# Performance work log

Hardware: AMD Instinct MI355X
Metric: run time of the kernel (lower is better)

The kernel has to match this reference:

```python
import jax, jax.numpy as jnp
import numpy as np

B, T, C = 4, 2048, 2048
H = 16
DH = C // H  # 128
ROPE_BASE = 10000.0


def _rms_norm(x):
    eps = jnp.finfo(x.dtype).eps
    return x * jax.lax.rsqrt(jnp.mean(x * x, axis=-1, keepdims=True) + eps)


def _rope_tables(seq_len, dim, dtype):
    inv_freq = 1.0 / (ROPE_BASE ** (jnp.arange(0, dim, 2, dtype=jnp.float32) / dim))
    t = jnp.arange(seq_len, dtype=jnp.float32)
    freqs = jnp.outer(t, inv_freq)  # [T, dim/2]
    return jnp.cos(freqs).astype(dtype), jnp.sin(freqs).astype(dtype)


def _apply_rotary(x, cos, sin):
    # x: [B, T, H, DH]; cos/sin: [T, DH/2] broadcast over batch and heads
    d = x.shape[-1] // 2
    x1, x2 = x[..., :d], x[..., d:]
    c = cos[None, :, None, :]
    s = sin[None, :, None, :]
    y1 = x1 * c + x2 * s
    y2 = -x1 * s + x2 * c
    return jnp.concatenate([y1, y2], axis=-1).astype(x.dtype)


def setup_inputs() -> dict:
    key = jax.random.key(0)
    k0, k1, k2, k3, k4 = jax.random.split(key, 5)
    scale = 1.0 / np.sqrt(C)
    return {
        "residual": jax.random.normal(k0, (B, T, C), dtype=jnp.float32),
        "wq": jax.random.normal(k1, (C, C), dtype=jnp.float32) * scale,
        "wk": jax.random.normal(k2, (C, C), dtype=jnp.float32) * scale,
        "wv": jax.random.normal(k3, (C, C), dtype=jnp.float32) * scale,
        "wproj": jax.random.normal(k4, (C, C), dtype=jnp.float32) * scale,
    }


def reference(residual, wq, wk, wv, wproj):
    x = _rms_norm(residual)  # [B, T, C]
    # torch Linear: y = x @ W.T, W is [out, in]
    q = jnp.einsum('btc,dc->btd', x, wq).reshape(B, T, H, DH)
    k = jnp.einsum('btc,dc->btd', x, wk).reshape(B, T, H, DH)
    v = jnp.einsum('btc,dc->btd', x, wv).reshape(B, T, H, DH)
    # per-head QK RMSNorm
    q = _rms_norm(q)
    k = _rms_norm(k)
    cos, sin = _rope_tables(T, DH, residual.dtype)
    q = _apply_rotary(q, cos, sin)
    k = _apply_rotary(k, cos, sin)
    # causal attention, scale 1/sqrt(head_dim)
    scores = jnp.einsum('bqhd,bkhd->bhqk', q, k) / jnp.sqrt(jnp.asarray(DH, q.dtype))
    causal = jnp.tril(jnp.ones((T, T), dtype=bool))
    scores = jnp.where(causal[None, None], scores, jnp.asarray(-jnp.inf, scores.dtype))
    attn = jax.nn.softmax(scores, axis=-1)
    y = jnp.einsum('bhqk,bkhd->bqhd', attn, v).reshape(B, T, C)
    y = jnp.einsum('btc,dc->btd', y, wproj)
    return residual + y
```

## Files before the change

### kernel.cpp

```cpp
#include <hip/hip_runtime.h>
#include <hip/hip_bf16.h>

#define B_  4
#define T_  2048
#define C_  2048
#define H_  16
#define DH_ 128
#define MROWS (B_ * T_)

typedef unsigned short bf16;
typedef __attribute__((ext_vector_type(8))) short bf16x8;
typedef __attribute__((ext_vector_type(4))) float f32x4;

__device__ __forceinline__ float bf2f(bf16 h) {
    return __uint_as_float(((unsigned int)h) << 16);
}
__device__ __forceinline__ bf16 f2bf(float f) {
    unsigned int u = __float_as_uint(f);
    u = (u + 0x7fffu + ((u >> 16) & 1u)) >> 16;
    return (bf16)u;
}

__device__ __forceinline__ int swz8(int row, int col) {
    return col ^ ((row & 7) << 3);
}

__device__ __forceinline__ void gld16(const bf16* g, bf16* l) {
    __builtin_amdgcn_global_load_lds(
        (const __attribute__((address_space(1))) unsigned int*)(const unsigned int*)g,
        (__attribute__((address_space(3))) unsigned int*)(unsigned int*)l,
        16, 0, 0);
}

__global__ __launch_bounds__(256) void w2bf(const float* __restrict__ w, bf16* __restrict__ o) {
    const size_t i = ((size_t)blockIdx.x * 256 + threadIdx.x) * 8;
    float4 a = *(const float4*)(w + i);
    float4 b = *(const float4*)(w + i + 4);
    union { uint4 u; bf16 h[8]; } p;
    p.h[0] = f2bf(a.x); p.h[1] = f2bf(a.y); p.h[2] = f2bf(a.z); p.h[3] = f2bf(a.w);
    p.h[4] = f2bf(b.x); p.h[5] = f2bf(b.y); p.h[6] = f2bf(b.z); p.h[7] = f2bf(b.w);
    *(uint4*)(o + i) = p.u;
}

__global__ __launch_bounds__(256) void rmsnorm_x(const float* __restrict__ in,
                                                 bf16* __restrict__ outx) {
    const int row = blockIdx.x, tid = threadIdx.x;
    const size_t base = (size_t)row * C_ + tid * 8;
    float4 a = *(const float4*)(in + base);
    float4 b = *(const float4*)(in + base + 4);
    float f[8] = {a.x, a.y, a.z, a.w, b.x, b.y, b.z, b.w};
    float ss = 0.f;
#pragma unroll
    for (int i = 0; i < 8; ++i) ss += f[i] * f[i];
#pragma unroll
    for (int m = 32; m; m >>= 1) ss += __shfl_xor(ss, m, 64);
    __shared__ float red[4];
    if ((tid & 63) == 0) red[tid >> 6] = ss;
    __syncthreads();
    float tot = red[0] + red[1] + red[2] + red[3];
    float sc = rsqrtf(tot * (1.0f / (float)C_) + 1.1920929e-07f);
    union { uint4 u; bf16 h[8]; } o;
#pragma unroll
    for (int i = 0; i < 8; ++i) o.h[i] = f2bf(f[i] * sc);
    *(uint4*)(outx + base) = o.u;
}

template <int MODE>
__global__ __launch_bounds__(256, 2)
void gemm_bt(const bf16* __restrict__ A, const bf16* __restrict__ W,
             void* __restrict__ Dv, const float* __restrict__ Add) {
    __shared__ __align__(16) bf16 sA[128 * 64];
    __shared__ __align__(16) bf16 sB[128 * 64];
    const int tid = threadIdx.x;
    const int w = tid >> 6, L = tid & 63;
    const int lane15 = L & 15, quad = L >> 4;
    const int m0 = blockIdx.x * 128, n0 = blockIdx.y * 128;
    const int wm = w >> 1, wn = w & 1;

    const bf16* aptr[4];
    const bf16* bptr[4];
#pragma unroll
    for (int it = 0; it < 4; ++it) {
        int slot = it * 256 + tid;
        int row = slot >> 3;
        int ch = slot & 7;
        aptr[it] = A + (size_t)(m0 + row) * C_ + ch * 8;
        bptr[it] = W + (size_t)(n0 + row) * C_ + ch * 8;
    }

    f32x4 acc[4][4] = {};
#pragma unroll 1
    for (int kt = 0; kt < C_ / 64; ++kt) {
        __syncthreads();
#pragma unroll
        for (int it = 0; it < 4; ++it) {
            gld16(aptr[it], sA + (size_t)(it * 256 + w * 64) * 8);
            aptr[it] += 64;
        }
#pragma unroll
        for (int it = 0; it < 4; ++it) {
            gld16(bptr[it], sB + (size_t)(it * 256 + w * 64) * 8);
            bptr[it] += 64;
        }
        __syncthreads();
#pragma unroll
        for (int ks = 0; ks < 2; ++ks) {
            bf16x8 af[4], bfr[4];
#pragma unroll
            for (int i = 0; i < 4; ++i) {
                int ar = wm * 64 + i * 16 + lane15;
                af[i]  = *(const bf16x8*)(sA + ar * 64 + (ks * 4 + quad) * 8);
                int br = wn * 64 + i * 16 + lane15;
                bfr[i] = *(const bf16x8*)(sB + br * 64 + (ks * 4 + quad) * 8);
            }
#pragma unroll
            for (int i = 0; i < 4; ++i)
#pragma unroll
                for (int j = 0; j < 4; ++j)
                    acc[i][j] = __builtin_amdgcn_mfma_f32_16x16x32_bf16(af[i], bfr[j], acc[i][j], 0, 0, 0);
        }
    }

    if (MODE == 2) {
        bf16* D = (bf16*)Dv;
#pragma unroll
        for (int i = 0; i < 4; ++i) {
            int t0 = m0 + wm * 64 + i * 16 + quad * 4;
            int bidx = t0 >> 11, tin = t0 & (T_ - 1);
#pragma unroll
            for (int j = 0; j < 4; ++j) {
                int col = n0 + wn * 64 + j * 16 + lane15;
                int hh = col >> 7, dh = col & (DH_ - 1);
                unsigned int lo = (unsigned int)f2bf(acc[i][j][0]) | ((unsigned int)f2bf(acc[i][j][1]) << 16);
                unsigned int hi = (unsigned int)f2bf(acc[i][j][2]) | ((unsigned int)f2bf(acc[i][j][3]) << 16);
                uint2 val; val.x = lo; val.y = hi;
                *(uint2*)(D + ((size_t)((bidx * H_ + hh) * DH_ + dh)) * T_ + tin) = val;
            }
        }
    } else if (MODE == 1) {
        float* D = (float*)Dv;
#pragma unroll
        for (int i = 0; i < 4; ++i)
#pragma unroll
            for (int j = 0; j < 4; ++j)
#pragma unroll
                for (int r = 0; r < 4; ++r) {
                    int row = m0 + wm * 64 + i * 16 + quad * 4 + r;
                    int col = n0 + wn * 64 + j * 16 + lane15;
                    D[(size_t)row * C_ + col] = acc[i][j][r] + Add[(size_t)row * C_ + col];
                }
    } else {
        bf16* D = (bf16*)Dv;
#pragma unroll
        for (int i = 0; i < 4; ++i)
#pragma unroll
            for (int j = 0; j < 4; ++j)
#pragma unroll
                for (int r = 0; r < 4; ++r) {
                    int row = m0 + wm * 64 + i * 16 + quad * 4 + r;
                    int col = n0 + wn * 64 + j * 16 + lane15;
                    D[(size_t)row * C_ + col] = f2bf(acc[i][j][r]);
                }
    }
}

__global__ __launch_bounds__(256) void qknorm_rope(bf16* __restrict__ q, bf16* __restrict__ k) {
    const int bt = blockIdx.x;
    bf16* buf = blockIdx.y ? k : q;
    const int w = threadIdx.x >> 6, L = threadIdx.x & 63;
    const int t = bt & (T_ - 1);
    float inv = (float)exp2(-(double)L * 0.20762050593046006);
    float ang = (float)t * inv;
    float s, c;
    sincosf(ang, &s, &c);
#pragma unroll
    for (int hh = 0; hh < 4; ++hh) {
        int h = w * 4 + hh;
        bf16* p = buf + (size_t)bt * C_ + h * DH_;
        float x1 = bf2f(p[L]), x2 = bf2f(p[L + 64]);
        float ss = x1 * x1 + x2 * x2;
#pragma unroll
        for (int m = 32; m; m >>= 1) ss += __shfl_xor(ss, m, 64);
        float sc = rsqrtf(ss * (1.0f / (float)DH_) + 1.1920929e-07f);
        float y1 = (x1 * c + x2 * s) * sc;
        float y2 = (x2 * c - x1 * s) * sc;
        p[L]      = f2bf(y1);
        p[L + 64] = f2bf(y2);
    }
}

__global__ __launch_bounds__(256, 2)
void attn_fwd(const bf16* __restrict__ q, const bf16* __restrict__ k,
              const bf16* __restrict__ vt, bf16* __restrict__ y) {
    __shared__ __align__(16) bf16 sK[2 * 64 * 128];
    __shared__ __align__(16) bf16 sV[2 * 128 * 64];
    __shared__ __align__(16) bf16 sP[128 * 64];
    const int qt = (int)gridDim.x - 1 - (int)blockIdx.x;
    const int bh = blockIdx.y;
    const int b = bh >> 4, h = bh & 15;
    const int tid = threadIdx.x;
    const int w = tid >> 6, L = tid & 63;
    const int lane15 = L & 15, quad = L >> 4;
    const float SCALE = 0.08838834764831845f;

    const bf16* kbase = k  + ((size_t)(b * T_)) * C_ + h * DH_;
    const bf16* vbase = vt + ((size_t)bh * DH_) * T_;

    bf16x8 qf[2][4];
#pragma unroll
    for (int nt = 0; nt < 2; ++nt)
#pragma unroll
        for (int ks = 0; ks < 4; ++ks) {
            int qrow = qt * 128 + w * 32 + nt * 16 + lane15;
            qf[nt][ks] = *(const bf16x8*)(q + ((size_t)(b * T_ + qrow)) * C_ + h * DH_ + ks * 32 + quad * 8);
        }

    f32x4 o[2][8] = {};
    float m_i[2] = {-__builtin_inff(), -__builtin_inff()};
    float l_i[2] = {0.f, 0.f};

    const int jlast = 2 * qt + 1;

#define STAGE_KV(jj, bi)                                                              \
    do {                                                                              \
        const int base_ = (jj) * 64;                                                  \
        _Pragma("unroll")                                                             \
        for (int it = 0; it < 4; ++it) {                                              \
            int slot = it * 256 + tid;                                                \
            int row = slot >> 4, ch = slot & 15;                                      \
            gld16(kbase + (size_t)(base_ + row) * C_ + ((ch ^ (row & 7)) << 3),       \
                  sK + (bi) * (64 * 128) + (size_t)(it * 256 + w * 64) * 8);          \
        }                                                                             \
        _Pragma("unroll")                                                             \
        for (int it = 0; it < 4; ++it) {                                              \
            int slot = it * 256 + tid;                                                \
            int row = slot >> 3, ch = slot & 7;                                       \
            gld16(vbase + (size_t)row * T_ + base_ + ((ch ^ (row & 7)) << 3),         \
                  sV + (bi) * (128 * 64) + (size_t)(it * 256 + w * 64) * 8);          \
        }                                                                             \
    } while (0)

    STAGE_KV(0, 0);
    __syncthreads();

    int cur = 0;
    for (int jj = 0; jj <= jlast; ++jj) {
        if (jj < jlast) STAGE_KV(jj + 1, cur ^ 1);

        const bool skip = (jj == jlast) && (w < 2);
        if (!skip) {
            const bf16* skc = sK + cur * (64 * 128);
            const bf16* svc = sV + cur * (128 * 64);

            f32x4 sc[4][2] = {};
            __builtin_amdgcn_s_setprio(1);
#pragma unroll
            for (int ks = 0; ks < 4; ++ks)
#pragma unroll
                for (int mt = 0; mt < 4; ++mt) {
                    int ar = mt * 16 + lane15;
                    bf16x8 a = *(const bf16x8*)(skc + ar * 128 + (((ks * 4 + quad) ^ (ar & 7)) << 3));
                    sc[mt][0] = __builtin_amdgcn_mfma_f32_16x16x32_bf16(a, qf[0][ks], sc[mt][0], 0, 0, 0);
                    sc[mt][1] = __builtin_amdgcn_mfma_f32_16x16x32_bf16(a, qf[1][ks], sc[mt][1], 0, 0, 0);
                }
            __builtin_amdgcn_s_setprio(0);

            const bool diag = (jj == 2 * qt && w < 2) || (jj == jlast && w >= 2);
            float alpha[2];
#pragma unroll
            for (int nt = 0; nt < 2; ++nt) {
                const int qr = qt * 128 + w * 32 + nt * 16 + lane15;
                float mx = -__builtin_inff();
#pragma unroll
                for (int mt = 0; mt < 4; ++mt)
#pragma unroll
                    for (int r = 0; r < 4; ++r) {
                        float v = sc[mt][nt][r] * SCALE;
                        if (diag) {
                            int kr = jj * 64 + mt * 16 + quad * 4 + r;
                            if (kr > qr) v = -__builtin_inff();
                        }
                        sc[mt][nt][r] = v;
                        mx = fmaxf(mx, v);
                    }
                mx = fmaxf(mx, __shfl_xor(mx, 16));
                mx = fmaxf(mx, __shfl_xor(mx, 32));
                float mn = fmaxf(m_i[nt], mx);
                alpha[nt] = __expf(m_i[nt] - mn);
                float sum = 0.f;
#pragma unroll
                for (int mt = 0; mt < 4; ++mt)
#pragma unroll
                    for (int r = 0; r < 4; ++r) {
                        float p = __expf(sc[mt][nt][r] - mn);
                        sc[mt][nt][r] = p;
                        sum += p;
                    }
                sum += __shfl_xor(sum, 16);
                sum += __shfl_xor(sum, 32);
                l_i[nt] = l_i[nt] * alpha[nt] + sum;
                m_i[nt] = mn;
            }

#pragma unroll
            for (int mt = 0; mt < 4; ++mt)
#pragma unroll
                for (int nt = 0; nt < 2; ++nt) {
                    int prow = w * 32 + nt * 16 + lane15;
                    int kr0 = mt * 16 + quad * 4;
                    int off = prow * 64 + ((((kr0 >> 3) ^ (prow & 7)) << 3) | (kr0 & 7));
                    unsigned int lo = (unsigned int)f2bf(sc[mt][nt][0]) | ((unsigned int)f2bf(sc[mt][nt][1]) << 16);
                    unsigned int hi = (unsigned int)f2bf(sc[mt][nt][2]) | ((unsigned int)f2bf(sc[mt][nt][3]) << 16);
                    uint2 val; val.x = lo; val.y = hi;
                    *(uint2*)(sP + off) = val;
                }

#pragma unroll
            for (int g = 0; g < 2; ++g)
#pragma unroll
                for (int r = 0; r < 4; ++r) {
                    float av = __shfl(alpha[g], quad * 4 + r, 64);
#pragma unroll
                    for (int d = 0; d < 8; ++d) o[g][d][r] *= av;
                }

            __builtin_amdgcn_s_setprio(1);
#pragma unroll
            for (int ks = 0; ks < 2; ++ks) {
                bf16x8 ap[2];
#pragma unroll
                for (int g = 0; g < 2; ++g) {
                    int pr = w * 32 + g * 16 + lane15;
                    ap[g] = *(const bf16x8*)(sP + pr * 64 + (((ks * 4 + quad) ^ (pr & 7)) << 3));
                }
#pragma unroll
                for (int d = 0; d < 8; ++d) {
                    int vr = d * 16 + lane15;
                    bf16x8 bv = *(const bf16x8*)(svc + vr * 64 + (((ks * 4 + quad) ^ (vr & 7)) << 3));
                    o[0][d] = __builtin_amdgcn_mfma_f32_16x16x32_bf16(ap[0], bv, o[0][d], 0, 0, 0);
                    o[1][d] = __builtin_amdgcn_mfma_f32_16x16x32_bf16(ap[1], bv, o[1][d], 0, 0, 0);
                }
            }
            __builtin_amdgcn_s_setprio(0);
        }

        __syncthreads();
        cur ^= 1;
    }
#undef STAGE_KV

    float rl[2] = {1.f / l_i[0], 1.f / l_i[1]};
#pragma unroll
    for (int g = 0; g < 2; ++g)
#pragma unroll
        for (int r = 0; r < 4; ++r) {
            float linv = __shfl(rl[g], quad * 4 + r, 64);
            int t = qt * 128 + w * 32 + g * 16 + quad * 4 + r;
#pragma unroll
            for (int d = 0; d < 8; ++d)
                y[((size_t)(b * T_ + t)) * C_ + h * DH_ + d * 16 + lane15] = f2bf(o[g][d][r] * linv);
        }
}

extern "C" void kernel_launch(void* const* d_in, const int* in_sizes, int n_in,
                              void* d_out, int out_size, void* d_ws, size_t ws_size,
                              hipStream_t stream) {
    const float* residual = (const float*)d_in[0];
    const float* wq    = (const float*)d_in[1];
    const float* wk    = (const float*)d_in[2];
    const float* wv    = (const float*)d_in[3];
    const float* wproj = (const float*)d_in[4];

    const size_t NE = (size_t)B_ * T_ * C_;
    const size_t WE = (size_t)C_ * C_;
    bf16* x  = (bf16*)d_ws;
    bf16* q  = x + NE;
    bf16* vt = q + NE;
    bf16* kk = (bf16*)d_out;
    bf16* wqb = kk + NE;
    bf16* wkb = wqb + WE;
    bf16* wvb = wkb + WE;
    bf16* y  = x;
    bf16* wpb = q;

    const dim3 gemm_grid(MROWS / 128, C_ / 128);
    const int wgrid = (int)(WE / (256 * 8));

    w2bf<<<wgrid, 256, 0, stream>>>(wq, wqb);
    w2bf<<<wgrid, 256, 0, stream>>>(wk, wkb);
    w2bf<<<wgrid, 256, 0, stream>>>(wv, wvb);
    rmsnorm_x<<<MROWS, 256, 0, stream>>>(residual, x);
    gemm_bt<0><<<gemm_grid, 256, 0, stream>>>(x, wqb, q,  nullptr);
    gemm_bt<0><<<gemm_grid, 256, 0, stream>>>(x, wkb, kk, nullptr);
    gemm_bt<2><<<gemm_grid, 256, 0, stream>>>(x, wvb, vt, nullptr);
    qknorm_rope<<<dim3(MROWS, 2), 256, 0, stream>>>(q, kk);
    attn_fwd<<<dim3(T_ / 128, B_ * H_), 256, 0, stream>>>(q, kk, vt, y);
    w2bf<<<wgrid, 256, 0, stream>>>(wproj, wpb);
    gemm_bt<1><<<gemm_grid, 256, 0, stream>>>(y, wpb, d_out, residual);
}
```

Measured before the change: 710.2 us.

## Single-buffer K/V tiles for higher occupancy and add lazy softmax rescaling

Drops the double-buffered K/V shared-memory staging in favour of a single buffer loaded synchronously each iteration, with syncs on both sides, and raises launch bounds to 3 blocks per CU. The smaller LDS footprint and register budget aim to fit more resident blocks so other blocks hide load latency. It also adds a lazy max update: the running max and output rescale are skipped unless a wave's new max exceeds the old one by more than 8, which trades some exp headroom for fewer multiplies. The cost is that K/V loads no longer overlap compute within a block, and register pressure may cause spills at the tighter bound.

```diff
diff --git a/kernel.cpp b/kernel.cpp
--- a/kernel.cpp
+++ b/kernel.cpp
@@ -189,11 +189,11 @@
     }
 }
 
-__global__ __launch_bounds__(256, 2)
+__global__ __launch_bounds__(256, 3)
 void attn_fwd(const bf16* __restrict__ q, const bf16* __restrict__ k,
               const bf16* __restrict__ vt, bf16* __restrict__ y) {
-    __shared__ __align__(16) bf16 sK[2 * 64 * 128];
-    __shared__ __align__(16) bf16 sV[2 * 128 * 64];
+    __shared__ __align__(16) bf16 sK[64 * 128];
+    __shared__ __align__(16) bf16 sV[128 * 64];
     __shared__ __align__(16) bf16 sP[128 * 64];
     const int qt = (int)gridDim.x - 1 - (int)blockIdx.x;
     const int bh = blockIdx.y;
@@ -221,7 +221,7 @@
 
     const int jlast = 2 * qt + 1;
 
-#define STAGE_KV(jj, bi)                                                              \
+#define STAGE_KV(jj)                                                                  \
     do {                                                                              \
         const int base_ = (jj) * 64;                                                  \
         _Pragma("unroll")                                                             \
@@ -229,29 +229,24 @@
             int slot = it * 256 + tid;                                                \
             int row = slot >> 4, ch = slot & 15;                                      \
             gld16(kbase + (size_t)(base_ + row) * C_ + ((ch ^ (row & 7)) << 3),       \
-                  sK + (bi) * (64 * 128) + (size_t)(it * 256 + w * 64) * 8);          \
+                  sK + (size_t)(it * 256 + w * 64) * 8);                              \
         }                                                                             \
         _Pragma("unroll")                                                             \
         for (int it = 0; it < 4; ++it) {                                              \
             int slot = it * 256 + tid;                                                \
             int row = slot >> 3, ch = slot & 7;                                       \
             gld16(vbase + (size_t)row * T_ + base_ + ((ch ^ (row & 7)) << 3),         \
-                  sV + (bi) * (128 * 64) + (size_t)(it * 256 + w * 64) * 8);          \
+                  sV + (size_t)(it * 256 + w * 64) * 8);                              \
         }                                                                             \
     } while (0)
 
-    STAGE_KV(0, 0);
-    __syncthreads();
-
-    int cur = 0;
     for (int jj = 0; jj <= jlast; ++jj) {
-        if (jj < jlast) STAGE_KV(jj + 1, cur ^ 1);
+        __syncthreads();
+        STAGE_KV(jj);
+        __syncthreads();
 
         const bool skip = (jj == jlast) && (w < 2);
         if (!skip) {
-            const bf16* skc = sK + cur * (64 * 128);
-            const bf16* svc = sV + cur * (128 * 64);
-
             f32x4 sc[4][2] = {};
             __builtin_amdgcn_s_setprio(1);
 #pragma unroll
@@ -259,7 +254,7 @@
 #pragma unroll
                 for (int mt = 0; mt < 4; ++mt) {
                     int ar = mt * 16 + lane15;
-                    bf16x8 a = *(const bf16x8*)(skc + ar * 128 + (((ks * 4 + quad) ^ (ar & 7)) << 3));
+                    bf16x8 a = *(const bf16x8*)(sK + ar * 128 + (((ks * 4 + quad) ^ (ar & 7)) << 3));
                     sc[mt][0] = __builtin_amdgcn_mfma_f32_16x16x32_bf16(a, qf[0][ks], sc[mt][0], 0, 0, 0);
                     sc[mt][1] = __builtin_amdgcn_mfma_f32_16x16x32_bf16(a, qf[1][ks], sc[mt][1], 0, 0, 0);
                 }
@@ -267,6 +262,7 @@
 
             const bool diag = (jj == 2 * qt && w < 2) || (jj == jlast && w >= 2);
             float alpha[2];
+            bool needv[2];
 #pragma unroll
             for (int nt = 0; nt < 2; ++nt) {
                 const int qr = qt * 128 + w * 32 + nt * 16 + lane15;
@@ -285,8 +281,10 @@
                     }
                 mx = fmaxf(mx, __shfl_xor(mx, 16));
                 mx = fmaxf(mx, __shfl_xor(mx, 32));
-                float mn = fmaxf(m_i[nt], mx);
-                alpha[nt] = __expf(m_i[nt] - mn);
+                bool nd = __any(mx > m_i[nt] + 8.0f) != 0;
+                float mn = nd ? fmaxf(m_i[nt], mx) : m_i[nt];
+                alpha[nt] = nd ? __expf(m_i[nt] - mn) : 1.0f;
+                needv[nt] = nd;
                 float sum = 0.f;
 #pragma unroll
                 for (int mt = 0; mt < 4; ++mt)
@@ -317,11 +315,13 @@
 
 #pragma unroll
             for (int g = 0; g < 2; ++g)
-#pragma unroll
-                for (int r = 0; r < 4; ++r) {
-                    float av = __shfl(alpha[g], quad * 4 + r, 64);
-#pragma unroll
-                    for (int d = 0; d < 8; ++d) o[g][d][r] *= av;
+                if (needv[g]) {
+#pragma unroll
+                    for (int r = 0; r < 4; ++r) {
+                        float av = __shfl(alpha[g], quad * 4 + r, 64);
+#pragma unroll
+                        for (int d = 0; d < 8; ++d) o[g][d][r] *= av;
+                    }
                 }
 
             __builtin_amdgcn_s_setprio(1);
@@ -336,16 +336,13 @@
 #pragma unroll
                 for (int d = 0; d < 8; ++d) {
                     int vr = d * 16 + lane15;
-                    bf16x8 bv = *(const bf16x8*)(svc + vr * 64 + (((ks * 4 + quad) ^ (vr & 7)) << 3));
+                    bf16x8 bv = *(const bf16x8*)(sV + vr * 64 + (((ks * 4 + quad) ^ (vr & 7)) << 3));
                     o[0][d] = __builtin_amdgcn_mfma_f32_16x16x32_bf16(ap[0], bv, o[0][d], 0, 0, 0);
                     o[1][d] = __builtin_amdgcn_mfma_f32_16x16x32_bf16(ap[1], bv, o[1][d], 0, 0, 0);
                 }
             }
             __builtin_amdgcn_s_setprio(0);
         }
-
-        __syncthreads();
-        cur ^= 1;
     }
 #undef STAGE_KV
 
```

After: 845.9 us. +19.1%, slower.
